# Performance work log

Hardware: AMD Instinct MI355X
Metric: run time of the kernel (lower is better)

Reference implementation:

```python
import jax, jax.numpy as jnp
import numpy as np
import math

B, C, H, W = 32, 256, 56, 56
M = 16            # num_frequency_mixtures
MIX = 4           # sqrt(M)
K = 8             # num_fourier_basis + 1
HID = 16
STRIDE = (1, 1)
EPS = 1e-5


def setup_inputs() -> dict:
    key = jax.random.key(0)
    ks = jax.random.split(key, 8)
    return {
        "x": jax.random.normal(ks[0], (B, C, H, W), jnp.float32),
        "fc1_w": jax.random.normal(ks[1], (HID, C), jnp.float32) * 0.08,
        "fc1_b": jnp.zeros((HID,), jnp.float32),
        "ln_g": jnp.ones((HID,), jnp.float32),
        "ln_b": jnp.zeros((HID,), jnp.float32),
        "fh_w": jax.random.normal(ks[2], (C * M * K, HID), jnp.float32) * 0.08,
        "fh_b": jnp.zeros((C * M * K,), jnp.float32),
        "basis_real": jax.random.normal(ks[3], (K, 56, 32), jnp.float32) * 0.5,
        "basis_imag": jax.random.normal(ks[4], (K, 56, 32), jnp.float32) * 0.5,
        "conv_w": jax.random.normal(ks[5], (C, C), jnp.float32) * (1.0 / math.sqrt(C)),
        "bn_g": jnp.ones((C,), jnp.float32),
        "bn_b": jnp.zeros((C,), jnp.float32),
    }


def reference(x, fc1_w, fc1_b, ln_g, ln_b, fh_w, fh_b,
              basis_real, basis_imag, conv_w, bn_g, bn_b):
    b, c, h, w = x.shape
    # --- FrequencyAttention: GAP -> fc1 -> LN -> ReLU -> fourier_head ---
    ctx = x.mean(axis=(2, 3))                          # (B, C)
    hdn = ctx @ fc1_w.T + fc1_b                        # (B, HID)
    mu = hdn.mean(-1, keepdims=True)
    var = hdn.var(-1, keepdims=True)
    hdn = (hdn - mu) / jnp.sqrt(var + EPS) * ln_g + ln_b
    hdn = jax.nn.relu(hdn)
    att = hdn @ fh_w.T + fh_b                          # (B, C*M*K)

    coeffs = jax.nn.softmax(att.reshape(b, c, M, K), axis=-1)  # (B,C,M,K)

    # --- work-canvas sizes ---
    h_out, w_out = h // STRIDE[0], w // STRIDE[1]
    h_work = math.ceil(h / MIX) * MIX                  # 56
    w_f = w // 2 + 1                                   # 29
    w_f_work = math.ceil(w_f / MIX) * MIX              # 32
    w_work = (w_f_work - 1) * 2 if w_f_work > 1 else 1 # 62

    if (h_work, w_work) != (h, w):
        x_work = jax.image.resize(x, (b, c, h_work, w_work), "bilinear")
    else:
        x_work = x

    x_ft = jnp.fft.rfft2(x_work, s=(h_work, w_work), norm="ortho")  # (B,C,Hw,Wfw) complex
    wf = x_ft.shape[-1]                                # == w_f_work
    ph, pwf = h_work // MIX, wf // MIX                 # 14, 8

    basis = jax.lax.complex(basis_real, basis_imag)    # (K, Hw, Wfw)
    basis_p = basis.reshape(K, MIX, ph, MIX, pwf).transpose(1, 3, 0, 2, 4)
    basis_p = basis_p.reshape(M, K, ph, pwf)           # (M,K,ph,pwf)

    x_ft_p = x_ft.reshape(b, c, MIX, ph, MIX, pwf).transpose(0, 2, 4, 1, 3, 5)
    x_ft_p = x_ft_p.reshape(b, M, c, ph, pwf)          # (B,M,C,ph,pwf)

    coeffs_c = jax.lax.complex(coeffs, jnp.zeros_like(coeffs))
    coeffs_p = coeffs_c.transpose(0, 2, 1, 3)          # (B,M,C,K)

    kernel = jnp.einsum("bmck,mkhw->bmchw", coeffs_p, basis_p)  # (B,M,C,ph,pwf)
    out_ft_p = x_ft_p * kernel

    out_ft = out_ft_p.reshape(b, MIX, MIX, c, ph, pwf).transpose(0, 3, 1, 4, 2, 5)
    out_ft = out_ft.reshape(b, c, h_work, wf)

    s_work = (h_work // STRIDE[0], w_work // STRIDE[1])
    y = jnp.fft.irfft2(out_ft, s=s_work, norm="ortho")  # (B,C,56,62)

    if y.shape[2:] != (h_out, w_out):
        y = jax.image.resize(y, (b, c, h_out, w_out), "bilinear")

    # --- 1x1 conv + BatchNorm (batch statistics, training-mode math) ---
    y = jnp.einsum("bchw,oc->bohw", y, conv_w)
    m = y.mean(axis=(0, 2, 3))
    v = y.var(axis=(0, 2, 3))
    y = (y - m[None, :, None, None]) / jnp.sqrt(v + EPS)[None, :, None, None]
    y = y * bn_g[None, :, None, None] + bn_b[None, :, None, None]
    return y
```

## Files before the change

### kernel.cpp

```cpp
#include <hip/hip_runtime.h>
#include <math.h>

typedef __attribute__((ext_vector_type(4))) float f32x4;
typedef __attribute__((ext_vector_type(8))) short s16x8;
typedef __attribute__((ext_vector_type(4))) short s16x4;
typedef unsigned short ushort_t;

#define MFMA16(a, b, c) __builtin_amdgcn_mfma_f32_16x16x32_bf16((a), (b), (c), 0, 0, 0)

#define WO_CTX    0u
#define WO_HDN    32768u
#define WO_BNSUM  34816u
#define WO_BNSQ   35840u
#define WO_SCALE  36864u
#define WO_SHIFT  37888u
#define WO_COEF   40960u
#define WO_BMT_H  4235264u
#define WO_BMT_L  4243456u
#define WO_FARE_H 4251648u
#define WO_FARE_L 4268032u
#define WO_FAIM_H 4284416u
#define WO_FAIM_L 4300800u
#define WO_FDRE_H 4317184u
#define WO_FDRE_L 4333568u
#define WO_FDIM_H 4349952u
#define WO_FDIM_L 4366336u
#define WO_DTT_H  4382720u
#define WO_DTT_L  4390912u
#define WO_CW_H   4399104u
#define WO_CW_L   4530176u
#define WO_YBF    4661248u
#define WO_BASRT  56041472u
#define WO_BASIT  56098816u

__device__ __forceinline__ ushort_t f2bf(float f) {
  unsigned int u = __builtin_bit_cast(unsigned int, f);
  unsigned int r = (u + 0x7fffu + ((u >> 16) & 1u)) >> 16;
  return (ushort_t)r;
}
__device__ __forceinline__ float bf2f(ushort_t h) {
  unsigned int u = ((unsigned int)h) << 16;
  return __builtin_bit_cast(float, u);
}

__device__ double bmat_val(int w, int vv) {
  const int v = vv & 31;
  const bool isI = vv >= 32;
  double accR = 0.0, accI = 0.0;
  for (int wp = 0; wp < 62; ++wp) {
    const double src = (wp + 0.5) * (56.0 / 62.0) - 0.5;
    const int w0 = (int)floor(src);
    const double f = src - (double)w0;
    const double s0 = (w0 >= 0 && w0 <= 55) ? (1.0 - f) : 0.0;
    const double s1 = (w0 + 1 >= 0 && w0 + 1 <= 55) ? f : 0.0;
    const double ssum = s0 + s1;
    double wgt = 0.0;
    if (w == w0) wgt = s0 / ssum;
    else if (w == w0 + 1) wgt = s1 / ssum;
    if (wgt != 0.0) {
      const int p = (v * wp) % 62;
      const double ang = 6.283185307179586476925286766559 * (double)p / 62.0;
      accR += wgt * cos(ang);
      accI -= wgt * sin(ang);
    }
  }
  const double nrm = 1.0 / sqrt(3472.0);
  return (isI ? accI : accR) * nrm;
}

__device__ double dt_component(int v, bool isI, int wq) {
  const double ks = 62.0 / 56.0;
  const double src = (wq + 0.5) * ks - 0.5;
  double wsum = 0.0;
  for (int wp = 0; wp < 62; ++wp) {
    const double xx = fabs(src - (double)wp) / ks;
    if (xx < 1.0) wsum += 1.0 - xx;
  }
  const double cv = (v == 0 || v == 31) ? 1.0 : 2.0;
  double accR = 0.0, accI = 0.0;
  for (int wp = 0; wp < 62; ++wp) {
    const double xx = fabs(src - (double)wp) / ks;
    if (xx >= 1.0) continue;
    const double wgt = (1.0 - xx) / wsum;
    double cc, ss;
    if (v == 0)       { cc = 1.0; ss = 0.0; }
    else if (v == 31) { cc = (wp & 1) ? -1.0 : 1.0; ss = 0.0; }
    else {
      const int p = (v * wp) % 62;
      const double ang = 6.283185307179586476925286766559 * (double)p / 62.0;
      cc = cos(ang); ss = sin(ang);
    }
    accR += wgt * cv * cc;
    accI -= wgt * cv * ss;
  }
  const double nrm = 1.0 / sqrt(3472.0);
  return (isI ? accI : accR) * nrm;
}

__device__ __forceinline__ void emit_hilo(ushort_t* hp, ushort_t* lp, int off, double val) {
  const float fv = (float)val;
  const ushort_t h = f2bf(fv);
  const float hf = bf2f(h);
  const ushort_t l = f2bf((float)(val - (double)hf));
  hp[off] = h;
  lp[off] = l;
}

__global__ void k_const(const float* __restrict__ conv_w,
                        const float* __restrict__ basR, const float* __restrict__ basI,
                        ushort_t* BmT_h, ushort_t* BmT_l,
                        ushort_t* FARe_h, ushort_t* FARe_l,
                        ushort_t* FAIm_h, ushort_t* FAIm_l,
                        ushort_t* FDRe_h, ushort_t* FDRe_l,
                        ushort_t* FDIm_h, ushort_t* FDIm_l,
                        ushort_t* DtT_h, ushort_t* DtT_l,
                        ushort_t* W_h, ushort_t* W_l,
                        float* basRT, float* basIT) {
  const int idx = blockIdx.x * 256 + threadIdx.x;
  if (idx < 4096) {
    const int vv = idx >> 6, k = idx & 63;
    const double v = (k < 56) ? bmat_val(k, vv) : 0.0;
    emit_hilo(BmT_h, BmT_l, idx, v);
  } else if (idx < 36864) {
    const int t = (idx - 4096) & 8191;
    const int which = (idx - 4096) >> 13;
    const int row = t >> 7, k = t & 127;
    double val = 0.0;
    if (row < 56 && k < 112) {
      const int h = (k < 56) ? k : k - 56;
      const double ang = 6.283185307179586476925286766559 *
                         (double)((row * h) % 56) / 56.0;
      const double c = cos(ang), s = sin(ang);
      const bool lowk = (k < 56);
      if (which == 0)      val = lowk ? c : s;
      else if (which == 1) val = lowk ? -s : c;
      else if (which == 2) val = lowk ? c : -s;
      else                 val = lowk ? s : c;
    }
    ushort_t* hp = (which == 0) ? FARe_h : (which == 1) ? FAIm_h : (which == 2) ? FDRe_h : FDIm_h;
    ushort_t* lp = (which == 0) ? FARe_l : (which == 1) ? FAIm_l : (which == 2) ? FDRe_l : FDIm_l;
    emit_hilo(hp, lp, t, val);
  } else if (idx < 40960) {
    const int t = idx - 36864;
    const int w = t >> 6, kk = t & 63;
    const double val = (w < 56) ? dt_component(kk >> 1, (kk & 1) != 0, w) : 0.0;
    emit_hilo(DtT_h, DtT_l, t, val);
  } else if (idx < 106496) {
    const int t = idx - 40960;
    emit_hilo(W_h, W_l, t, (double)conv_w[t]);
  } else if (idx < 135168) {
    const int t = idx - 106496;
    const int mat = t >> 14;
    const int tt = t - (t / 14336) * 14336;
    const int m2 = t / 14336;
    const int q = tt >> 3, k = tt & 7;
    if (m2 == 0) basRT[tt] = basR[k * 1792 + q];
    else         basIT[tt] = basI[k * 1792 + q];
    (void)mat;
  }
}

__global__ __launch_bounds__(256) void k_gap(const float* __restrict__ x,
                                             float* __restrict__ ctx) {
  const int img = blockIdx.x;
  const int tid = threadIdx.x;
  const float4* p4 = (const float4*)(x + (size_t)img * 3136);
  float s = 0.f;
  for (int i = tid; i < 784; i += 256) {
    const float4 v = p4[i];
    s += v.x + v.y + v.z + v.w;
  }
  for (int off = 32; off > 0; off >>= 1) s += __shfl_down(s, off, 64);
  __shared__ float ls[4];
  if ((tid & 63) == 0) ls[tid >> 6] = s;
  __syncthreads();
  if (tid == 0) ctx[img] = (ls[0] + ls[1] + ls[2] + ls[3]) * (1.0f / 3136.0f);
}

__global__ void k_mlp(const float* __restrict__ ctx, const float* __restrict__ fc1_w,
                      const float* __restrict__ fc1_b, const float* __restrict__ ln_g,
                      const float* __restrict__ ln_b, float* __restrict__ hdn) {
  const int b = blockIdx.x;
  const int j = threadIdx.x;
  __shared__ float h[16];
  if (j < 16) {
    const float* cr = ctx + b * 256;
    const float* wr = fc1_w + j * 256;
    float acc = fc1_b[j];
    for (int c0 = 0; c0 < 256; ++c0) acc = fmaf(cr[c0], wr[c0], acc);
    h[j] = acc;
  }
  __syncthreads();
  if (j < 16) {
    float mu = 0.f, m2 = 0.f;
    for (int t = 0; t < 16; ++t) { mu += h[t]; m2 += h[t] * h[t]; }
    mu *= 0.0625f; m2 *= 0.0625f;
    const float var = m2 - mu * mu;
    const float val = (h[j] - mu) / sqrtf(var + 1e-5f) * ln_g[j] + ln_b[j];
    hdn[b * 16 + j] = fmaxf(val, 0.f);
  }
}

__global__ __launch_bounds__(256) void k_coeffs(const float* __restrict__ hdn,
                                                const float* __restrict__ fh_w,
                                                const float* __restrict__ fh_b,
                                                float* __restrict__ coeffs) {
  const int gid = blockIdx.x * 256 + threadIdx.x;
  const int b = gid >> 12;
  const int cm = gid & 4095;
  float hv[16];
  const float* hp = hdn + b * 16;
#pragma unroll
  for (int j = 0; j < 16; ++j) hv[j] = hp[j];
  const int row0 = cm * 8;
  float a[8];
  float mx = -1e30f;
#pragma unroll
  for (int k = 0; k < 8; ++k) {
    const float* wr = fh_w + (size_t)(row0 + k) * 16;
    float acc = fh_b[row0 + k];
#pragma unroll
    for (int j = 0; j < 16; ++j) acc = fmaf(hv[j], wr[j], acc);
    a[k] = acc;
    mx = fmaxf(mx, acc);
  }
  float s = 0.f;
#pragma unroll
  for (int k = 0; k < 8; ++k) { a[k] = expf(a[k] - mx); s += a[k]; }
  const float inv = 1.f / s;
  float* outp = coeffs + (size_t)gid * 8;
#pragma unroll
  for (int k = 0; k < 8; ++k) outp[k] = a[k] * inv;
}

__global__ __launch_bounds__(256) void k_fft(
    const float* __restrict__ x, const float* __restrict__ coeffs,
    const float* __restrict__ basRT, const float* __restrict__ basIT,
    const ushort_t* __restrict__ BmT_h, const ushort_t* __restrict__ BmT_l,
    const ushort_t* __restrict__ FARe_h, const ushort_t* __restrict__ FARe_l,
    const ushort_t* __restrict__ FAIm_h, const ushort_t* __restrict__ FAIm_l,
    const ushort_t* __restrict__ FDRe_h, const ushort_t* __restrict__ FDRe_l,
    const ushort_t* __restrict__ FDIm_h, const ushort_t* __restrict__ FDIm_l,
    const ushort_t* __restrict__ DtT_h, const ushort_t* __restrict__ DtT_l,
    ushort_t* __restrict__ ybf) {
  __shared__ __align__(16) ushort_t xta[64 * 72];
  __shared__ __align__(16) ushort_t x1T[32 * 136];
  __shared__ __align__(16) ushort_t x2T[32 * 136];
  __shared__ float gf[3584];
  const int img = blockIdx.x;
  const int tid = threadIdx.x;
  const int wave = tid >> 6, lane = tid & 63, col = lane & 15, quad = lane >> 4;
  const f32x4 zf = {0.f, 0.f, 0.f, 0.f};

  for (int i = tid; i < 224; i += 256) {
    const int h = i >> 2, c = i & 3;
    *(unsigned int*)&xta[h * 72 + 56 + c * 2] = 0u;
  }
  for (int i = tid; i < 512; i += 256) {
    const int r = (i >> 3) & 31, c = i & 7;
    ushort_t* bp = (i < 256) ? x1T : x2T;
    *(unsigned int*)&bp[r * 136 + 112 + c * 2] = 0u;
  }
  {
    const float4* xp = (const float4*)(x + (size_t)img * 3136);
    for (int f = tid; f < 784; f += 256) {
      const float4 v = xp[f];
      const int h = f / 14, w4 = (f % 14) * 4;
      s16x4 p;
      p[0] = (short)f2bf(v.x); p[1] = (short)f2bf(v.y);
      p[2] = (short)f2bf(v.z); p[3] = (short)f2bf(v.w);
      *(s16x4*)&xta[h * 72 + w4] = p;
    }
    const float* co = coeffs + (size_t)img * 128;
#pragma unroll
    for (int g = 0; g < 4; ++g) {
      const int m = g * 4 + ((tid & 31) >> 3);
      const float4 c0 = *(const float4*)&co[m * 8];
      const float4 c1 = *(const float4*)&co[m * 8 + 4];
#pragma unroll
      for (int i2 = 0; i2 < 2; ++i2) {
        if (i2 == 1 && tid >= 192) continue;
        const int qq = g * 448 + i2 * 256 + tid;
        const float4 br0 = *(const float4*)&basRT[qq * 8];
        const float4 br1 = *(const float4*)&basRT[qq * 8 + 4];
        const float4 bi0 = *(const float4*)&basIT[qq * 8];
        const float4 bi1 = *(const float4*)&basIT[qq * 8 + 4];
        float gr = 0.f, gi = 0.f;
        gr = fmaf(c0.x, br0.x, gr); gi = fmaf(c0.x, bi0.x, gi);
        gr = fmaf(c0.y, br0.y, gr); gi = fmaf(c0.y, bi0.y, gi);
        gr = fmaf(c0.z, br0.z, gr); gi = fmaf(c0.z, bi0.z, gi);
        gr = fmaf(c0.w, br0.w, gr); gi = fmaf(c0.w, bi0.w, gi);
        gr = fmaf(c1.x, br1.x, gr); gi = fmaf(c1.x, bi1.x, gi);
        gr = fmaf(c1.y, br1.y, gr); gi = fmaf(c1.y, bi1.y, gi);
        gr = fmaf(c1.z, br1.z, gr); gi = fmaf(c1.z, bi1.z, gi);
        gr = fmaf(c1.w, br1.w, gr); gi = fmaf(c1.w, bi1.w, gi);
        gf[qq] = gr;
        gf[1792 + qq] = gi;
      }
    }
  }
  __syncthreads();

  {
    const int mt = wave;
    const int arow = (mt * 16 + col) * 72;
    const s16x8 a0 = *(const s16x8*)&xta[arow + quad * 8];
    const s16x8 a1 = *(const s16x8*)&xta[arow + 32 + quad * 8];
    const int h0 = mt * 16 + quad * 4;
    for (int nt = 0; nt < 4; ++nt) {
      const int nrow = nt * 16 + col;
      const s16x8 bh0 = *(const s16x8*)&BmT_h[nrow * 64 + quad * 8];
      const s16x8 bl0 = *(const s16x8*)&BmT_l[nrow * 64 + quad * 8];
      const s16x8 bh1 = *(const s16x8*)&BmT_h[nrow * 64 + 32 + quad * 8];
      const s16x8 bl1 = *(const s16x8*)&BmT_l[nrow * 64 + 32 + quad * 8];
      f32x4 acc = zf;
      acc = MFMA16(a0, bh0, acc);
      acc = MFMA16(a0, bl0, acc);
      acc = MFMA16(a1, bh1, acc);
      acc = MFMA16(a1, bl1, acc);
      if (h0 < 56) {
        s16x4 p;
        p[0] = (short)f2bf(acc[0]); p[1] = (short)f2bf(acc[1]);
        p[2] = (short)f2bf(acc[2]); p[3] = (short)f2bf(acc[3]);
        const int vr = nrow & 31;
        const int kk = (nrow < 32) ? h0 : 56 + h0;
        *(s16x4*)&x1T[vr * 136 + kk] = p;
      }
    }
  }
  __syncthreads();

  {
    const int mt = wave;
    f32x4 accRe[2] = {zf, zf}, accIm[2] = {zf, zf};
    for (int ks = 0; ks < 4; ++ks) {
      const int aoff = (mt * 16 + col) * 128 + ks * 32 + quad * 8;
      const s16x8 aRh = *(const s16x8*)&FARe_h[aoff];
      const s16x8 aRl = *(const s16x8*)&FARe_l[aoff];
      const s16x8 aIh = *(const s16x8*)&FAIm_h[aoff];
      const s16x8 aIl = *(const s16x8*)&FAIm_l[aoff];
#pragma unroll
      for (int nt = 0; nt < 2; ++nt) {
        const s16x8 b = *(const s16x8*)&x1T[(nt * 16 + col) * 136 + ks * 32 + quad * 8];
        accRe[nt] = MFMA16(aRh, b, accRe[nt]);
        accRe[nt] = MFMA16(aRl, b, accRe[nt]);
        accIm[nt] = MFMA16(aIh, b, accIm[nt]);
        accIm[nt] = MFMA16(aIl, b, accIm[nt]);
      }
    }
    const int u0 = mt * 16 + quad * 4;
    if (u0 < 56) {
#pragma unroll
      for (int nt = 0; nt < 2; ++nt) {
        const int v = nt * 16 + col;
        s16x4 pR, pI;
#pragma unroll
        for (int r = 0; r < 4; ++r) {
          const int u = u0 + r;
          const float gr = gf[u * 32 + v];
          const float gi = gf[1792 + u * 32 + v];
          const float re = accRe[nt][r] * gr - accIm[nt][r] * gi;
          const float im = accRe[nt][r] * gi + accIm[nt][r] * gr;
          pR[r] = (short)f2bf(re);
          pI[r] = (short)f2bf(im);
        }
        *(s16x4*)&x2T[v * 136 + u0] = pR;
        *(s16x4*)&x2T[v * 136 + 56 + u0] = pI;
      }
    }
  }
  __syncthreads();

  {
    const int mt = wave;
    f32x4 accRe[2] = {zf, zf}, accIm[2] = {zf, zf};
    for (int ks = 0; ks < 4; ++ks) {
      const int aoff = (mt * 16 + col) * 128 + ks * 32 + quad * 8;
      const s16x8 aRh = *(const s16x8*)&FDRe_h[aoff];
      const s16x8 aRl = *(const s16x8*)&FDRe_l[aoff];
      const s16x8 aIh = *(const s16x8*)&FDIm_h[aoff];
      const s16x8 aIl = *(const s16x8*)&FDIm_l[aoff];
#pragma unroll
      for (int nt = 0; nt < 2; ++nt) {
        const s16x8 b = *(const s16x8*)&x2T[(nt * 16 + col) * 136 + ks * 32 + quad * 8];
        accRe[nt] = MFMA16(aRh, b, accRe[nt]);
        accRe[nt] = MFMA16(aRl, b, accRe[nt]);
        accIm[nt] = MFMA16(aIh, b, accIm[nt]);
        accIm[nt] = MFMA16(aIl, b, accIm[nt]);
      }
    }
    const int h0 = mt * 16 + quad * 4;
#pragma unroll
    for (int nt = 0; nt < 2; ++nt) {
      const int v = nt * 16 + col;
#pragma unroll
      for (int r = 0; r < 4; ++r) {
        const unsigned int pk = (unsigned int)f2bf(accRe[nt][r]) |
                                ((unsigned int)f2bf(accIm[nt][r]) << 16);
        *(unsigned int*)&xta[(h0 + r) * 72 + 2 * v] = pk;
      }
    }
  }
  __syncthreads();

  {
    const int mt = wave;
    const int arow = (mt * 16 + col) * 72;
    const s16x8 a0 = *(const s16x8*)&xta[arow + quad * 8];
    const s16x8 a1 = *(const s16x8*)&xta[arow + 32 + quad * 8];
    const int h0 = mt * 16 + quad * 4;
    ushort_t* yo = ybf + (size_t)img * 3136;
    for (int nt = 0; nt < 4; ++nt) {
      const int w = nt * 16 + col;
      const s16x8 bh0 = *(const s16x8*)&DtT_h[w * 64 + quad * 8];
      const s16x8 bl0 = *(const s16x8*)&DtT_l[w * 64 + quad * 8];
      const s16x8 bh1 = *(const s16x8*)&DtT_h[w * 64 + 32 + quad * 8];
      const s16x8 bl1 = *(const s16x8*)&DtT_l[w * 64 + 32 + quad * 8];
      f32x4 acc = zf;
      acc = MFMA16(a0, bh0, acc);
      acc = MFMA16(a0, bl0, acc);
      acc = MFMA16(a1, bh1, acc);
      acc = MFMA16(a1, bl1, acc);
      if (h0 < 56 && w < 56) {
#pragma unroll
        for (int r = 0; r < 4; ++r) yo[(h0 + r) * 56 + w] = f2bf(acc[r]);
      }
    }
  }
}

__global__ __launch_bounds__(256) void k_conv(const ushort_t* __restrict__ ybf,
                                              const ushort_t* __restrict__ W_h,
                                              const ushort_t* __restrict__ W_l,
                                              float* __restrict__ z) {
  const int pb = blockIdx.x;
  const int oh = blockIdx.y;
  const int b = blockIdx.z;
  const int tid = threadIdx.x;
  const int wave = tid >> 6, lane = tid & 63, col = lane & 15, quad = lane >> 4;
  const f32x4 zf = {0.f, 0.f, 0.f, 0.f};
  f32x4 acc[8][4];
#pragma unroll
  for (int mt = 0; mt < 8; ++mt)
#pragma unroll
    for (int i = 0; i < 4; ++i) acc[mt][i] = zf;

  const size_t ybase = (size_t)b * 256 * 3136;
  int p0i[4];
  bool act[4];
#pragma unroll
  for (int i = 0; i < 4; ++i) {
    p0i[i] = pb * 256 + (wave * 4 + i) * 16;
    act[i] = p0i[i] < 3136;
  }

  for (int ks = 0; ks < 8; ++ks) {
    const int c0 = ks * 32 + quad * 8;
    s16x8 bfr[4];
#pragma unroll
    for (int i = 0; i < 4; ++i) {
      if (act[i]) {
        s16x8 t;
#pragma unroll
        for (int j = 0; j < 8; ++j)
          t[j] = (short)ybf[ybase + (size_t)(c0 + j) * 3136 + p0i[i] + col];
        bfr[i] = t;
      }
    }
#pragma unroll
    for (int mt = 0; mt < 8; ++mt) {
      const int orow = oh * 128 + mt * 16 + col;
      const s16x8 ah = *(const s16x8*)&W_h[orow * 256 + ks * 32 + quad * 8];
      const s16x8 al = *(const s16x8*)&W_l[orow * 256 + ks * 32 + quad * 8];
#pragma unroll
      for (int i = 0; i < 4; ++i) {
        if (act[i]) {
          acc[mt][i] = MFMA16(ah, bfr[i], acc[mt][i]);
          acc[mt][i] = MFMA16(al, bfr[i], acc[mt][i]);
        }
      }
    }
  }

#pragma unroll
  for (int mt = 0; mt < 8; ++mt) {
#pragma unroll
    for (int i = 0; i < 4; ++i) {
      if (!act[i]) continue;
#pragma unroll
      for (int r = 0; r < 4; ++r) {
        const int o = oh * 128 + mt * 16 + quad * 4 + r;
        z[((size_t)b * 256 + o) * 3136 + p0i[i] + col] = acc[mt][i][r];
      }
    }
  }
}

__global__ __launch_bounds__(256) void k_bnsum(const float* __restrict__ z,
                                               float* __restrict__ bnsum,
                                               float* __restrict__ bnsq) {
  const int bo = blockIdx.x;
  const int tid = threadIdx.x;
  const float4* p4 = (const float4*)(z + (size_t)bo * 3136);
  float s = 0.f, s2 = 0.f;
  for (int i = tid; i < 784; i += 256) {
    const float4 v = p4[i];
    s += v.x + v.y + v.z + v.w;
    s2 += v.x * v.x + v.y * v.y + v.z * v.z + v.w * v.w;
  }
  for (int off = 32; off > 0; off >>= 1) {
    s += __shfl_down(s, off, 64);
    s2 += __shfl_down(s2, off, 64);
  }
  __shared__ float ls[8];
  if ((tid & 63) == 0) { ls[tid >> 6] = s; ls[4 + (tid >> 6)] = s2; }
  __syncthreads();
  if (tid == 0) {
    atomicAdd(bnsum + (bo & 255), ls[0] + ls[1] + ls[2] + ls[3]);
    atomicAdd(bnsq + (bo & 255), ls[4] + ls[5] + ls[6] + ls[7]);
  }
}

__global__ void k_bnstats(const float* __restrict__ bnsum, const float* __restrict__ bnsq,
                          const float* __restrict__ bn_g, const float* __restrict__ bn_b,
                          float* __restrict__ scale, float* __restrict__ shift) {
  const int o = threadIdx.x;
  if (o < 256) {
    const float N = 32.f * 3136.f;
    const float m = bnsum[o] / N;
    const float v = bnsq[o] / N - m * m;
    const float sc = bn_g[o] / sqrtf(v + 1e-5f);
    scale[o] = sc;
    shift[o] = bn_b[o] - m * sc;
  }
}

__global__ __launch_bounds__(256) void k_bnapply(float* __restrict__ z,
                                                 const float* __restrict__ scale,
                                                 const float* __restrict__ shift) {
  const size_t i = ((size_t)blockIdx.x * 256 + threadIdx.x) * 4;
  const int ch = (int)((i / 3136) & 255);
  const float sc = scale[ch], sh = shift[ch];
  float4 v = *(float4*)(z + i);
  v.x = fmaf(v.x, sc, sh);
  v.y = fmaf(v.y, sc, sh);
  v.z = fmaf(v.z, sc, sh);
  v.w = fmaf(v.w, sc, sh);
  *(float4*)(z + i) = v;
}

extern "C" void kernel_launch(void* const* d_in, const int* in_sizes, int n_in,
                              void* d_out, int out_size, void* d_ws, size_t ws_size,
                              hipStream_t stream) {
  const float* x          = (const float*)d_in[0];
  const float* fc1_w      = (const float*)d_in[1];
  const float* fc1_b      = (const float*)d_in[2];
  const float* ln_g       = (const float*)d_in[3];
  const float* ln_b       = (const float*)d_in[4];
  const float* fh_w       = (const float*)d_in[5];
  const float* fh_b       = (const float*)d_in[6];
  const float* basis_real = (const float*)d_in[7];
  const float* basis_imag = (const float*)d_in[8];
  const float* conv_w     = (const float*)d_in[9];
  const float* bn_g       = (const float*)d_in[10];
  const float* bn_b       = (const float*)d_in[11];
  float* out = (float*)d_out;
  char* ws = (char*)d_ws;
  (void)in_sizes; (void)n_in; (void)out_size; (void)ws_size;

  float* ctx   = (float*)(ws + WO_CTX);
  float* hdn   = (float*)(ws + WO_HDN);
  float* bnsum = (float*)(ws + WO_BNSUM);
  float* bnsq  = (float*)(ws + WO_BNSQ);
  float* scale = (float*)(ws + WO_SCALE);
  float* shift = (float*)(ws + WO_SHIFT);
  float* coef  = (float*)(ws + WO_COEF);
  ushort_t* BmT_h  = (ushort_t*)(ws + WO_BMT_H);
  ushort_t* BmT_l  = (ushort_t*)(ws + WO_BMT_L);
  ushort_t* FARe_h = (ushort_t*)(ws + WO_FARE_H);
  ushort_t* FARe_l = (ushort_t*)(ws + WO_FARE_L);
  ushort_t* FAIm_h = (ushort_t*)(ws + WO_FAIM_H);
  ushort_t* FAIm_l = (ushort_t*)(ws + WO_FAIM_L);
  ushort_t* FDRe_h = (ushort_t*)(ws + WO_FDRE_H);
  ushort_t* FDRe_l = (ushort_t*)(ws + WO_FDRE_L);
  ushort_t* FDIm_h = (ushort_t*)(ws + WO_FDIM_H);
  ushort_t* FDIm_l = (ushort_t*)(ws + WO_FDIM_L);
  ushort_t* DtT_h  = (ushort_t*)(ws + WO_DTT_H);
  ushort_t* DtT_l  = (ushort_t*)(ws + WO_DTT_L);
  ushort_t* W_h    = (ushort_t*)(ws + WO_CW_H);
  ushort_t* W_l    = (ushort_t*)(ws + WO_CW_L);
  ushort_t* ybf    = (ushort_t*)(ws + WO_YBF);
  float* basRT = (float*)(ws + WO_BASRT);
  float* basIT = (float*)(ws + WO_BASIT);

  hipMemsetAsync(bnsum, 0, 2048, stream);

  hipLaunchKernelGGL(k_const, dim3(528), dim3(256), 0, stream,
                     conv_w, basis_real, basis_imag,
                     BmT_h, BmT_l, FARe_h, FARe_l, FAIm_h, FAIm_l,
                     FDRe_h, FDRe_l, FDIm_h, FDIm_l, DtT_h, DtT_l, W_h, W_l,
                     basRT, basIT);
  hipLaunchKernelGGL(k_gap, dim3(8192), dim3(256), 0, stream, x, ctx);
  hipLaunchKernelGGL(k_mlp, dim3(32), dim3(64), 0, stream,
                     ctx, fc1_w, fc1_b, ln_g, ln_b, hdn);
  hipLaunchKernelGGL(k_coeffs, dim3(512), dim3(256), 0, stream, hdn, fh_w, fh_b, coef);
  hipLaunchKernelGGL(k_fft, dim3(8192), dim3(256), 0, stream,
                     x, coef, basRT, basIT,
                     BmT_h, BmT_l, FARe_h, FARe_l, FAIm_h, FAIm_l,
                     FDRe_h, FDRe_l, FDIm_h, FDIm_l, DtT_h, DtT_l, ybf);
  hipLaunchKernelGGL(k_conv, dim3(13, 2, 32), dim3(256), 0, stream, ybf, W_h, W_l, out);
  hipLaunchKernelGGL(k_bnsum, dim3(8192), dim3(256), 0, stream, out, bnsum, bnsq);
  hipLaunchKernelGGL(k_bnstats, dim3(1), dim3(256), 0, stream,
                     bnsum, bnsq, bn_g, bn_b, scale, shift);
  hipLaunchKernelGGL(k_bnapply, dim3(25088), dim3(256), 0, stream, out, scale, shift);
}
```

Measured before the change: 699.1 us.

## Run FFT kernel as single-wave blocks with ping-pong LDS and fused spectral filter

Each per-image FFT block now runs as one 64-lane wave that loops over the four row tiles instead of four waves sharing the work. Shared memory shrinks from four buffers plus a float filter array to two ping-pong buffers. The spectral filter is computed directly inside the multiply stage from coefficients and transposed basis, rather than staged through LDS first. The aim is lower LDS use per block, more resident blocks, and cheaper barriers, at the cost of less parallelism inside each block and more global/L2 loads for the basis and coefficients per wave.

```diff
diff --git a/kernel.cpp b/kernel.cpp
--- a/kernel.cpp
+++ b/kernel.cpp
@@ -150,13 +150,11 @@
     emit_hilo(W_h, W_l, t, (double)conv_w[t]);
   } else if (idx < 135168) {
     const int t = idx - 106496;
-    const int mat = t >> 14;
     const int tt = t - (t / 14336) * 14336;
     const int m2 = t / 14336;
     const int q = tt >> 3, k = tt & 7;
     if (m2 == 0) basRT[tt] = basR[k * 1792 + q];
     else         basIT[tt] = basI[k * 1792 + q];
-    (void)mat;
   }
 }
 
@@ -233,7 +231,7 @@
   for (int k = 0; k < 8; ++k) outp[k] = a[k] * inv;
 }
 
-__global__ __launch_bounds__(256) void k_fft(
+__global__ __launch_bounds__(64) void k_fft(
     const float* __restrict__ x, const float* __restrict__ coeffs,
     const float* __restrict__ basRT, const float* __restrict__ basIT,
     const ushort_t* __restrict__ BmT_h, const ushort_t* __restrict__ BmT_l,
@@ -243,70 +241,47 @@
     const ushort_t* __restrict__ FDIm_h, const ushort_t* __restrict__ FDIm_l,
     const ushort_t* __restrict__ DtT_h, const ushort_t* __restrict__ DtT_l,
     ushort_t* __restrict__ ybf) {
-  __shared__ __align__(16) ushort_t xta[64 * 72];
-  __shared__ __align__(16) ushort_t x1T[32 * 136];
-  __shared__ __align__(16) ushort_t x2T[32 * 136];
-  __shared__ float gf[3584];
+  __shared__ __align__(16) ushort_t regA[4608];
+  __shared__ __align__(16) ushort_t regB[4608];
   const int img = blockIdx.x;
-  const int tid = threadIdx.x;
-  const int wave = tid >> 6, lane = tid & 63, col = lane & 15, quad = lane >> 4;
+  const int lane = threadIdx.x;
+  const int col = lane & 15, quad = lane >> 4;
   const f32x4 zf = {0.f, 0.f, 0.f, 0.f};
 
-  for (int i = tid; i < 224; i += 256) {
-    const int h = i >> 2, c = i & 3;
-    *(unsigned int*)&xta[h * 72 + 56 + c * 2] = 0u;
-  }
-  for (int i = tid; i < 512; i += 256) {
-    const int r = (i >> 3) & 31, c = i & 7;
-    ushort_t* bp = (i < 256) ? x1T : x2T;
-    *(unsigned int*)&bp[r * 136 + 112 + c * 2] = 0u;
-  }
   {
+#pragma unroll
+    for (int i = 0; i < 4; ++i) {
+      const int t = i * 64 + lane;
+      if (t < 224) {
+        const int h = t >> 2, c = t & 3;
+        *(unsigned int*)&regA[h * 72 + 56 + c * 2] = 0u;
+      }
+    }
+#pragma unroll
+    for (int i = 0; i < 4; ++i) {
+      const int t = i * 64 + lane;
+      const int r = t >> 3, c = t & 7;
+      *(unsigned int*)&regB[r * 136 + 112 + c * 2] = 0u;
+    }
     const float4* xp = (const float4*)(x + (size_t)img * 3136);
-    for (int f = tid; f < 784; f += 256) {
+    for (int f = lane; f < 784; f += 64) {
       const float4 v = xp[f];
       const int h = f / 14, w4 = (f % 14) * 4;
       s16x4 p;
       p[0] = (short)f2bf(v.x); p[1] = (short)f2bf(v.y);
       p[2] = (short)f2bf(v.z); p[3] = (short)f2bf(v.w);
-      *(s16x4*)&xta[h * 72 + w4] = p;
-    }
-    const float* co = coeffs + (size_t)img * 128;
-#pragma unroll
-    for (int g = 0; g < 4; ++g) {
-      const int m = g * 4 + ((tid & 31) >> 3);
-      const float4 c0 = *(const float4*)&co[m * 8];
-      const float4 c1 = *(const float4*)&co[m * 8 + 4];
-#pragma unroll
-      for (int i2 = 0; i2 < 2; ++i2) {
-        if (i2 == 1 && tid >= 192) continue;
-        const int qq = g * 448 + i2 * 256 + tid;
-        const float4 br0 = *(const float4*)&basRT[qq * 8];
-        const float4 br1 = *(const float4*)&basRT[qq * 8 + 4];
-        const float4 bi0 = *(const float4*)&basIT[qq * 8];
-        const float4 bi1 = *(const float4*)&basIT[qq * 8 + 4];
-        float gr = 0.f, gi = 0.f;
-        gr = fmaf(c0.x, br0.x, gr); gi = fmaf(c0.x, bi0.x, gi);
-        gr = fmaf(c0.y, br0.y, gr); gi = fmaf(c0.y, bi0.y, gi);
-        gr = fmaf(c0.z, br0.z, gr); gi = fmaf(c0.z, bi0.z, gi);
-        gr = fmaf(c0.w, br0.w, gr); gi = fmaf(c0.w, bi0.w, gi);
-        gr = fmaf(c1.x, br1.x, gr); gi = fmaf(c1.x, bi1.x, gi);
-        gr = fmaf(c1.y, br1.y, gr); gi = fmaf(c1.y, bi1.y, gi);
-        gr = fmaf(c1.z, br1.z, gr); gi = fmaf(c1.z, bi1.z, gi);
-        gr = fmaf(c1.w, br1.w, gr); gi = fmaf(c1.w, bi1.w, gi);
-        gf[qq] = gr;
-        gf[1792 + qq] = gi;
-      }
+      *(s16x4*)&regA[h * 72 + w4] = p;
     }
   }
   __syncthreads();
 
-  {
-    const int mt = wave;
+#pragma unroll
+  for (int mt = 0; mt < 4; ++mt) {
     const int arow = (mt * 16 + col) * 72;
-    const s16x8 a0 = *(const s16x8*)&xta[arow + quad * 8];
-    const s16x8 a1 = *(const s16x8*)&xta[arow + 32 + quad * 8];
+    const s16x8 a0 = *(const s16x8*)&regA[arow + quad * 8];
+    const s16x8 a1 = *(const s16x8*)&regA[arow + 32 + quad * 8];
     const int h0 = mt * 16 + quad * 4;
+#pragma unroll
     for (int nt = 0; nt < 4; ++nt) {
       const int nrow = nt * 16 + col;
       const s16x8 bh0 = *(const s16x8*)&BmT_h[nrow * 64 + quad * 8];
@@ -324,56 +299,82 @@
         p[2] = (short)f2bf(acc[2]); p[3] = (short)f2bf(acc[3]);
         const int vr = nrow & 31;
         const int kk = (nrow < 32) ? h0 : 56 + h0;
-        *(s16x4*)&x1T[vr * 136 + kk] = p;
+        *(s16x4*)&regB[vr * 136 + kk] = p;
       }
     }
   }
   __syncthreads();
 
   {
-    const int mt = wave;
+#pragma unroll
+    for (int i = 0; i < 4; ++i) {
+      const int t = i * 64 + lane;
+      const int r = t >> 3, c = t & 7;
+      *(unsigned int*)&regA[r * 136 + 112 + c * 2] = 0u;
+    }
+    const float* co = coeffs + (size_t)img * 128;
+#pragma unroll
+    for (int mt = 0; mt < 4; ++mt) {
+      f32x4 accRe[2] = {zf, zf}, accIm[2] = {zf, zf};
+#pragma unroll
+      for (int ks = 0; ks < 4; ++ks) {
+        const int aoff = (mt * 16 + col) * 128 + ks * 32 + quad * 8;
+        const s16x8 aRh = *(const s16x8*)&FARe_h[aoff];
+        const s16x8 aRl = *(const s16x8*)&FARe_l[aoff];
+        const s16x8 aIh = *(const s16x8*)&FAIm_h[aoff];
+        const s16x8 aIl = *(const s16x8*)&FAIm_l[aoff];
+#pragma unroll
+        for (int nt = 0; nt < 2; ++nt) {
+          const s16x8 b = *(const s16x8*)&regB[(nt * 16 + col) * 136 + ks * 32 + quad * 8];
+          accRe[nt] = MFMA16(aRh, b, accRe[nt]);
+          accRe[nt] = MFMA16(aRl, b, accRe[nt]);
+          accIm[nt] = MFMA16(aIh, b, accIm[nt]);
+          accIm[nt] = MFMA16(aIl, b, accIm[nt]);
+        }
+      }
+      const int u0 = mt * 16 + quad * 4;
+      if (u0 < 56) {
+#pragma unroll
+        for (int nt = 0; nt < 2; ++nt) {
+          const int v = nt * 16 + col;
+          s16x4 pR, pI;
+#pragma unroll
+          for (int r = 0; r < 4; ++r) {
+            const int u = u0 + r;
+            const int q = u * 32 + v;
+            const int m = (u / 14) * 4 + (v >> 3);
+            const float4 c0 = *(const float4*)&co[m * 8];
+            const float4 c1 = *(const float4*)&co[m * 8 + 4];
+            const float4 br0 = *(const float4*)&basRT[q * 8];
+            const float4 br1 = *(const float4*)&basRT[q * 8 + 4];
+            const float4 bi0 = *(const float4*)&basIT[q * 8];
+            const float4 bi1 = *(const float4*)&basIT[q * 8 + 4];
+            float gr = 0.f, gi = 0.f;
+            gr = fmaf(c0.x, br0.x, gr); gi = fmaf(c0.x, bi0.x, gi);
+            gr = fmaf(c0.y, br0.y, gr); gi = fmaf(c0.y, bi0.y, gi);
+            gr = fmaf(c0.z, br0.z, gr); gi = fmaf(c0.z, bi0.z, gi);
+            gr = fmaf(c0.w, br0.w, gr); gi = fmaf(c0.w, bi0.w, gi);
+            gr = fmaf(c1.x, br1.x, gr); gi = fmaf(c1.x, bi1.x, gi);
+            gr = fmaf(c1.y, br1.y, gr); gi = fmaf(c1.y, bi1.y, gi);
+            gr = fmaf(c1.z, br1.z, gr); gi = fmaf(c1.z, bi1.z, gi);
+            gr = fmaf(c1.w, br1.w, gr); gi = fmaf(c1.w, bi1.w, gi);
+            const float re = accRe[nt][r] * gr - accIm[nt][r] * gi;
+            const float im = accRe[nt][r] * gi + accIm[nt][r] * gr;
+            pR[r] = (short)f2bf(re);
+            pI[r] = (short)f2bf(im);
+          }
+          *(s16x4*)&regA[v * 136 + u0] = pR;
+          *(s16x4*)&regA[v * 136 + 56 + u0] = pI;
+        }
+      }
+    }
+  }
+  __syncthreads();
+
+#pragma unroll
+  for (int mt = 0; mt < 4; ++mt) {
     f32x4 accRe[2] = {zf, zf}, accIm[2] = {zf, zf};
-    for (int ks = 0; ks < 4; ++ks) {
-      const int aoff = (mt * 16 + col) * 128 + ks * 32 + quad * 8;
-      const s16x8 aRh = *(const s16x8*)&FARe_h[aoff];
-      const s16x8 aRl = *(const s16x8*)&FARe_l[aoff];
-      const s16x8 aIh = *(const s16x8*)&FAIm_h[aoff];
-      const s16x8 aIl = *(const s16x8*)&FAIm_l[aoff];
-#pragma unroll
-      for (int nt = 0; nt < 2; ++nt) {
-        const s16x8 b = *(const s16x8*)&x1T[(nt * 16 + col) * 136 + ks * 32 + quad * 8];
-        accRe[nt] = MFMA16(aRh, b, accRe[nt]);
-        accRe[nt] = MFMA16(aRl, b, accRe[nt]);
-        accIm[nt] = MFMA16(aIh, b, accIm[nt]);
-        accIm[nt] = MFMA16(aIl, b, accIm[nt]);
-      }
-    }
-    const int u0 = mt * 16 + quad * 4;
-    if (u0 < 56) {
-#pragma unroll
-      for (int nt = 0; nt < 2; ++nt) {
-        const int v = nt * 16 + col;
-        s16x4 pR, pI;
-#pragma unroll
-        for (int r = 0; r < 4; ++r) {
-          const int u = u0 + r;
-          const float gr = gf[u * 32 + v];
-          const float gi = gf[1792 + u * 32 + v];
-          const float re = accRe[nt][r] * gr - accIm[nt][r] * gi;
-          const float im = accRe[nt][r] * gi + accIm[nt][r] * gr;
-          pR[r] = (short)f2bf(re);
-          pI[r] = (short)f2bf(im);
-        }
-        *(s16x4*)&x2T[v * 136 + u0] = pR;
-        *(s16x4*)&x2T[v * 136 + 56 + u0] = pI;
-      }
-    }
-  }
-  __syncthreads();
-
-  {
-    const int mt = wave;
-    f32x4 accRe[2] = {zf, zf}, accIm[2] = {zf, zf};
+#pragma unroll
     for (int ks = 0; ks < 4; ++ks) {
       const int aoff = (mt * 16 + col) * 128 + ks * 32 + quad * 8;
       const s16x8 aRh = *(const s16x8*)&FDRe_h[aoff];
@@ -382,7 +383,7 @@
       const s16x8 aIl = *(const s16x8*)&FDIm_l[aoff];
 #pragma unroll
       for (int nt = 0; nt < 2; ++nt) {
-        const s16x8 b = *(const s16x8*)&x2T[(nt * 16 + col) * 136 + ks * 32 + quad * 8];
+        const s16x8 b = *(const s16x8*)&regA[(nt * 16 + col) * 136 + ks * 32 + quad * 8];
         accRe[nt] = MFMA16(aRh, b, accRe[nt]);
         accRe[nt] = MFMA16(aRl, b, accRe[nt]);
         accIm[nt] = MFMA16(aIh, b, accIm[nt]);
@@ -397,33 +398,36 @@
       for (int r = 0; r < 4; ++r) {
         const unsigned int pk = (unsigned int)f2bf(accRe[nt][r]) |
                                 ((unsigned int)f2bf(accIm[nt][r]) << 16);
-        *(unsigned int*)&xta[(h0 + r) * 72 + 2 * v] = pk;
+        *(unsigned int*)&regB[(h0 + r) * 72 + 2 * v] = pk;
       }
     }
   }
   __syncthreads();
 
   {
-    const int mt = wave;
-    const int arow = (mt * 16 + col) * 72;
-    const s16x8 a0 = *(const s16x8*)&xta[arow + quad * 8];
-    const s16x8 a1 = *(const s16x8*)&xta[arow + 32 + quad * 8];
-    const int h0 = mt * 16 + quad * 4;
     ushort_t* yo = ybf + (size_t)img * 3136;
-    for (int nt = 0; nt < 4; ++nt) {
-      const int w = nt * 16 + col;
-      const s16x8 bh0 = *(const s16x8*)&DtT_h[w * 64 + quad * 8];
-      const s16x8 bl0 = *(const s16x8*)&DtT_l[w * 64 + quad * 8];
-      const s16x8 bh1 = *(const s16x8*)&DtT_h[w * 64 + 32 + quad * 8];
-      const s16x8 bl1 = *(const s16x8*)&DtT_l[w * 64 + 32 + quad * 8];
-      f32x4 acc = zf;
-      acc = MFMA16(a0, bh0, acc);
-      acc = MFMA16(a0, bl0, acc);
-      acc = MFMA16(a1, bh1, acc);
-      acc = MFMA16(a1, bl1, acc);
-      if (h0 < 56 && w < 56) {
-#pragma unroll
-        for (int r = 0; r < 4; ++r) yo[(h0 + r) * 56 + w] = f2bf(acc[r]);
+#pragma unroll
+    for (int mt = 0; mt < 4; ++mt) {
+      const int arow = (mt * 16 + col) * 72;
+      const s16x8 a0 = *(const s16x8*)&regB[arow + quad * 8];
+      const s16x8 a1 = *(const s16x8*)&regB[arow + 32 + quad * 8];
+      const int h0 = mt * 16 + quad * 4;
+#pragma unroll
+      for (int nt = 0; nt < 4; ++nt) {
+        const int w = nt * 16 + col;
+        const s16x8 bh0 = *(const s16x8*)&DtT_h[w * 64 + quad * 8];
+        const s16x8 bl0 = *(const s16x8*)&DtT_l[w * 64 + quad * 8];
+        const s16x8 bh1 = *(const s16x8*)&DtT_h[w * 64 + 32 + quad * 8];
+        const s16x8 bl1 = *(const s16x8*)&DtT_l[w * 64 + 32 + quad * 8];
+        f32x4 acc = zf;
+        acc = MFMA16(a0, bh0, acc);
+        acc = MFMA16(a0, bl0, acc);
+        acc = MFMA16(a1, bh1, acc);
+        acc = MFMA16(a1, bl1, acc);
+        if (h0 < 56 && w < 56) {
+#pragma unroll
+          for (int r = 0; r < 4; ++r) yo[(h0 + r) * 56 + w] = f2bf(acc[r]);
+        }
       }
     }
   }
@@ -604,7 +608,7 @@
   hipLaunchKernelGGL(k_mlp, dim3(32), dim3(64), 0, stream,
                      ctx, fc1_w, fc1_b, ln_g, ln_b, hdn);
   hipLaunchKernelGGL(k_coeffs, dim3(512), dim3(256), 0, stream, hdn, fh_w, fh_b, coef);
-  hipLaunchKernelGGL(k_fft, dim3(8192), dim3(256), 0, stream,
+  hipLaunchKernelGGL(k_fft, dim3(8192), dim3(64), 0, stream,
                      x, coef, basRT, basIT,
                      BmT_h, BmT_l, FARe_h, FARe_l, FAIm_h, FAIm_l,
                      FDRe_h, FDRe_l, FDIm_h, FDIm_l, DtT_h, DtT_l, ybf);
```

Measured after the change: 634.4 us. 1.1x faster.
